# Optimization experiments

Hardware: AMD Instinct MI355X
Metric: run time of the kernel (lower is better)

The kernel has to match this reference:

```python
import jax, jax.numpy as jnp
import numpy as np

B, P1, P2 = 32, 25, 24          # batch, patch rows (+1 cls row), patch cols
D1, D2, D3 = 8, 8, 12           # factored embed dims (total d = 768)
H1, H2, H3 = 2, 2, 4            # factored heads (16 total)
X, Y, Z = D1 // H1, D2 // H2, D3 // H3   # per-head factor dims -> head dim 48
SCALE = float((X * Y * Z) ** -0.5)


def tle(x, w1, w2, w3, b):
    # Tensor Linear Embedding: mode-wise linear maps on the last 3 modes + bias.
    return jnp.einsum('bpqijk,ai,cj,dk->bpqacd', x, w1, w2, w3) + b


def split_heads(t):
    # (b,p1,p2,(x h1),(y h2),(z h3)) -> (b,h1,h2,h3, p1*p2, x*y*z)
    b, p1, p2, _, _, _ = t.shape
    t = t.reshape(b, p1, p2, X, H1, Y, H2, Z, H3)
    t = t.transpose(0, 4, 6, 8, 1, 2, 3, 5, 7)
    return t.reshape(b, H1, H2, H3, p1 * p2, X * Y * Z)


def merge_heads(t, p1, p2):
    # (b,h1,h2,h3,S,D) -> (b,p1,p2,(x h1),(y h2),(z h3))
    b = t.shape[0]
    t = t.reshape(b, H1, H2, H3, p1, p2, X, Y, Z)
    t = t.transpose(0, 4, 5, 6, 1, 7, 2, 8, 3)
    return t.reshape(b, p1, p2, X * H1, Y * H2, Z * H3)


def setup_inputs() -> dict:
    key = jax.random.key(0)
    ks = jax.random.split(key, 20)

    def w(k, shape):
        return jax.random.normal(k, shape, jnp.float32) * 0.02

    inp = {"x": jax.random.normal(ks[0], (B, P1, P2, D1, D2, D3), jnp.float32)}
    for i, n in enumerate(["q", "k", "v", "o"]):
        inp[f"w{n}1"] = w(ks[1 + 4 * i], (D1, D1))
        inp[f"w{n}2"] = w(ks[2 + 4 * i], (D2, D2))
        inp[f"w{n}3"] = w(ks[3 + 4 * i], (D3, D3))
        inp[f"b{n}"] = w(ks[4 + 4 * i], (D1, D2, D3))
    return inp


def reference(x, wq1, wq2, wq3, bq, wk1, wk2, wk3, bk,
              wv1, wv2, wv3, bv, wo1, wo2, wo3, bo):
    q = split_heads(tle(x, wq1, wq2, wq3, bq))
    k = split_heads(tle(x, wk1, wk2, wk3, bk))
    v = split_heads(tle(x, wv1, wv2, wv3, bv))
    # scores: (b,h1,h2,h3,S,S) with S = 600
    attn = jax.nn.softmax(jnp.einsum('befgsd,befgtd->befgst', q, k) * SCALE, axis=-1)
    o = jnp.einsum('befgst,befgtd->befgsd', attn, v)
    o = merge_heads(o, P1, P2)
    return tle(o, wo1, wo2, wo3, bo)
```

## Files before the change

kernel.cpp:

```cpp
#include <hip/hip_runtime.h>
#include <hip/hip_bf16.h>
#include <cstdint>

#define Bc    32
#define Sc    600
#define NHc   16
#define SP    640
#define NKT   19
#define DHc   48
#define DP    64
#define SCALEc 0.14433756729740643f

typedef __bf16   bf16x8 __attribute__((ext_vector_type(8)));
typedef float    f32x4  __attribute__((ext_vector_type(4)));
typedef float    f32x16 __attribute__((ext_vector_type(16)));
typedef uint32_t u32x4  __attribute__((ext_vector_type(4)));

static __device__ __forceinline__ f32x16 mfma32(bf16x8 a, bf16x8 b, f32x16 c) {
    return __builtin_amdgcn_mfma_f32_32x32x16_bf16(a, b, c, 0, 0, 0);
}
static __device__ __forceinline__ unsigned short f2bf(float f) {
    uint32_t u = __builtin_bit_cast(uint32_t, f);
    u += 0x7FFFu + ((u >> 16) & 1u);
    return (unsigned short)(u >> 16);
}
static __device__ __forceinline__ f32x16 fzero16() {
    f32x16 z;
    #pragma unroll
    for (int i = 0; i < 16; ++i) z[i] = 0.f;
    return z;
}
static __device__ __forceinline__ void gload_lds16(const void* g, void* l) {
    __builtin_amdgcn_global_load_lds(
        (const __attribute__((address_space(1))) unsigned int*)g,
        (__attribute__((address_space(3))) unsigned int*)l, 16, 0, 0);
}

__global__ __launch_bounds__(256) void tle_qkv(
    const float* __restrict__ x,
    const float* __restrict__ wq1, const float* __restrict__ wq2,
    const float* __restrict__ wq3, const float* __restrict__ bq,
    const float* __restrict__ wk1, const float* __restrict__ wk2,
    const float* __restrict__ wk3, const float* __restrict__ bk,
    const float* __restrict__ wv1, const float* __restrict__ wv2,
    const float* __restrict__ wv3, const float* __restrict__ bv,
    __hip_bfloat16* __restrict__ Qb, __hip_bfloat16* __restrict__ Kb,
    __hip_bfloat16* __restrict__ Vr)
{
    __shared__ __align__(16) float xs[768];
    __shared__ __align__(16) float t1s[3][8][100];
    __shared__ __align__(16) float w3s[3][144];
    __shared__ __align__(16) unsigned short outs[3][16][64];
    const int t = threadIdx.x;
    const int patch = blockIdx.x;
    const int b = patch / Sc, s = patch - b * Sc;
    if (t < 192) ((float4*)xs)[t] = ((const float4*)(x + (size_t)patch * 768))[t];
    if (t < 144) { w3s[0][t] = wq3[t]; w3s[1][t] = wk3[t]; w3s[2][t] = wv3[t]; }
    __syncthreads();

    const int pr = t >> 6, a = (t >> 3) & 7, c = t & 7;
    float w2r[8];
    if (t < 192) {
        const float* w1 = pr == 0 ? wq1 : pr == 1 ? wk1 : wv1;
        const float* w2 = pr == 0 ? wq2 : pr == 1 ? wk2 : wv2;
        float w1r[8];
        #pragma unroll
        for (int i = 0; i < 8; ++i) w1r[i] = w1[a*8 + i];
        #pragma unroll
        for (int j = 0; j < 8; ++j) w2r[j] = w2[c*8 + j];
        float s1[12];
        #pragma unroll
        for (int k = 0; k < 12; ++k) s1[k] = 0.f;
        #pragma unroll
        for (int i = 0; i < 8; ++i) {
            const float4* xr = (const float4*)&xs[i*96 + c*12];
            float4 v0 = xr[0], v1 = xr[1], v2 = xr[2];
            float wv = w1r[i];
            s1[0] += wv*v0.x; s1[1] += wv*v0.y; s1[2]  += wv*v0.z; s1[3]  += wv*v0.w;
            s1[4] += wv*v1.x; s1[5] += wv*v1.y; s1[6]  += wv*v1.z; s1[7]  += wv*v1.w;
            s1[8] += wv*v2.x; s1[9] += wv*v2.y; s1[10] += wv*v2.z; s1[11] += wv*v2.w;
        }
        float4* tw = (float4*)&t1s[pr][a][c*12];
        tw[0] = make_float4(s1[0], s1[1], s1[2],  s1[3]);
        tw[1] = make_float4(s1[4], s1[5], s1[6],  s1[7]);
        tw[2] = make_float4(s1[8], s1[9], s1[10], s1[11]);
    }
    __syncthreads();
    if (t < 192) {
        float t2r[12];
        #pragma unroll
        for (int k = 0; k < 12; ++k) t2r[k] = 0.f;
        #pragma unroll
        for (int j = 0; j < 8; ++j) {
            const float4* tr = (const float4*)&t1s[pr][a][j*12];
            float4 v0 = tr[0], v1 = tr[1], v2 = tr[2];
            float wv = w2r[j];
            t2r[0] += wv*v0.x; t2r[1] += wv*v0.y; t2r[2]  += wv*v0.z; t2r[3]  += wv*v0.w;
            t2r[4] += wv*v1.x; t2r[5] += wv*v1.y; t2r[6]  += wv*v1.z; t2r[7]  += wv*v1.w;
            t2r[8] += wv*v2.x; t2r[9] += wv*v2.y; t2r[10] += wv*v2.z; t2r[11] += wv*v2.w;
        }
        const float* bb = pr == 0 ? bq : pr == 1 ? bk : bv;
        const float4* bp = (const float4*)(bb + a*96 + c*12);
        float4 b0 = bp[0], b1 = bp[1], b2 = bp[2];
        float bias_[12] = {b0.x,b0.y,b0.z,b0.w, b1.x,b1.y,b1.z,b1.w, b2.x,b2.y,b2.z,b2.w};
        #pragma unroll
        for (int d = 0; d < 12; ++d) {
            const float4* wr = (const float4*)&w3s[pr][d*12];
            float4 u0 = wr[0], u1 = wr[1], u2 = wr[2];
            float od = bias_[d]
                + t2r[0]*u0.x + t2r[1]*u0.y + t2r[2] *u0.z + t2r[3] *u0.w
                + t2r[4]*u1.x + t2r[5]*u1.y + t2r[6] *u1.z + t2r[7] *u1.w
                + t2r[8]*u2.x + t2r[9]*u2.y + t2r[10]*u2.z + t2r[11]*u2.w;
            if (pr == 0) od *= SCALEc;
            int h  = (a & 1)*8 + (c & 1)*4 + (d & 3);
            int dh = (a >> 1)*12 + (c >> 1)*3 + (d >> 2);
            outs[pr][h][dh] = f2bf(od);
        }
    }
    if (t < 96) {
        int prr = t >> 5, rem = t & 31, h = rem >> 1, half = rem & 1;
        *(uint4*)&outs[prr][h][48 + half*8] = make_uint4(0u, 0u, 0u, 0u);
    }
    __syncthreads();
    for (int u = t; u < 384; u += 256) {
        int prr = u >> 7, rem = u & 127, h = rem >> 3, u8 = rem & 7;
        __hip_bfloat16* dstp = prr == 0 ? Qb : prr == 1 ? Kb : Vr;
        uint4 v = *(const uint4*)&outs[prr][h][u8*8];
        *(uint4*)(dstp + ((size_t)(b*NHc + h) * SP + s) * DP + u8*8) = v;
    }
}

__global__ __launch_bounds__(256) void vtrans(
    const __hip_bfloat16* __restrict__ Vr, __hip_bfloat16* __restrict__ Vt,
    __hip_bfloat16* __restrict__ Kb)
{
    __shared__ __align__(16) short Ls[64][72];
    const int t = threadIdx.x;
    const int bh = blockIdx.x, st = blockIdx.y;
    const __hip_bfloat16* src = Vr + ((size_t)bh * SP + st*64) * DP;
    for (int u = t; u < 512; u += 256) {
        int r = u >> 3, c = (u & 7) * 8;
        *(bf16x8*)&Ls[r][c] = *(const bf16x8*)(src + (size_t)r * DP + c);
    }
    __syncthreads();
    const unsigned short one_bf = 0x3F80;
    for (int u = t; u < 384; u += 256) {
        int dh = u >> 3, cb = (u & 7) * 8;
        int gcol = st*64 + cb;
        if (gcol >= Sc + 8) continue;
        union { unsigned short s[8]; bf16x8 v; } o;
        if (gcol >= Sc) {
            #pragma unroll
            for (int j = 0; j < 8; ++j) o.s[j] = 0;
        } else {
            #pragma unroll
            for (int j = 0; j < 8; ++j) o.s[j] = (unsigned short)Ls[cb + j][dh];
        }
        *(bf16x8*)(Vt + ((size_t)bh*64 + dh) * SP + st*64 + cb) = o.v;
    }
    if (t < 128) {
        int r = 48 + (t >> 3), cb = (t & 7) * 8;
        union { unsigned short s[8]; bf16x8 v; } o;
        #pragma unroll
        for (int j = 0; j < 8; ++j) {
            int col = st*64 + cb + j;
            o.s[j] = (r == 48 && col < Sc) ? one_bf : (unsigned short)0;
        }
        *(bf16x8*)(Vt + ((size_t)bh*64 + r) * SP + st*64 + cb) = o.v;
    }
    if (st == 9 && t < 64) {
        int r = 600 + (t >> 3), cb = (t & 7) * 8;
        union { unsigned short s[8]; bf16x8 v; } z;
        #pragma unroll
        for (int j = 0; j < 8; ++j) z.s[j] = 0;
        *(bf16x8*)(Kb + ((size_t)bh * SP + r) * DP + cb) = z.v;
    }
}

static __device__ __forceinline__ void softmax_pack(
    const f32x16& sv, bf16x8& pf0, bf16x8& pf1)
{
    float p[16];
    #pragma unroll
    for (int r = 0; r < 16; ++r) p[r] = __expf(sv[r]);
    uint32_t Wa0, Wa1, Wa2, Wa3, Wb0, Wb1, Wb2, Wb3;
    asm("v_cvt_pk_bf16_f32 %0, %1, %2" : "=v"(Wa0) : "v"(p[0]),  "v"(p[1]));
    asm("v_cvt_pk_bf16_f32 %0, %1, %2" : "=v"(Wb0) : "v"(p[2]),  "v"(p[3]));
    asm("v_cvt_pk_bf16_f32 %0, %1, %2" : "=v"(Wa1) : "v"(p[4]),  "v"(p[5]));
    asm("v_cvt_pk_bf16_f32 %0, %1, %2" : "=v"(Wb1) : "v"(p[6]),  "v"(p[7]));
    asm("v_cvt_pk_bf16_f32 %0, %1, %2" : "=v"(Wa2) : "v"(p[8]),  "v"(p[9]));
    asm("v_cvt_pk_bf16_f32 %0, %1, %2" : "=v"(Wb2) : "v"(p[10]), "v"(p[11]));
    asm("v_cvt_pk_bf16_f32 %0, %1, %2" : "=v"(Wa3) : "v"(p[12]), "v"(p[13]));
    asm("v_cvt_pk_bf16_f32 %0, %1, %2" : "=v"(Wb3) : "v"(p[14]), "v"(p[15]));
    asm("v_permlane32_swap_b32 %0, %1" : "+v"(Wa0), "+v"(Wa1));
    asm("v_permlane32_swap_b32 %0, %1" : "+v"(Wb0), "+v"(Wb1));
    asm("v_permlane32_swap_b32 %0, %1" : "+v"(Wa2), "+v"(Wa3));
    asm("v_permlane32_swap_b32 %0, %1" : "+v"(Wb2), "+v"(Wb3));
    pf0 = __builtin_bit_cast(bf16x8, (u32x4){Wa0, Wb0, Wa1, Wb1});
    pf1 = __builtin_bit_cast(bf16x8, (u32x4){Wa2, Wb2, Wa3, Wb3});
}

__global__ __launch_bounds__(64, 2) void attn_mfma(
    const __hip_bfloat16* __restrict__ Qb, const __hip_bfloat16* __restrict__ Kb,
    const __hip_bfloat16* __restrict__ Vt, float* __restrict__ Ob)
{
    __shared__ __align__(16) char Ks[2][4096];
    __shared__ __align__(16) char Vs[2][4096];
    const int l = threadIdx.x;
    const int q32 = l & 31, hl = l >> 5;
    const int bid = blockIdx.x;
    const int lg = (bid & 7) * 320 + (bid >> 3);
    const int bh = lg / 5, qb = lg - bh * 5;
    const int b = bh >> 4, h = bh & 15;

    const char* Kbh = (const char*)(Kb + (size_t)bh * SP * DP);
    const char* Vbh = (const char*)(Vt + (size_t)bh * 64 * SP);

    const int krow = l >> 3;
    const char* ksrc = Kbh + krow*128 + (((l & 7)*16) ^ (krow << 4));
    const char* vsrc = Vbh + (size_t)(l >> 2)*(SP*2) + (l & 3)*16;

    bf16x8 qf[4][3];
    #pragma unroll
    for (int f = 0; f < 4; ++f) {
        const __hip_bfloat16* Qp = Qb + ((size_t)bh*SP + qb*128 + f*32 + q32) * DP;
        #pragma unroll
        for (int ck = 0; ck < 3; ++ck)
            qf[f][ck] = *(const bf16x8*)(Qp + ck*16 + hl*8);
    }
    f32x16 acc[4][2];
    #pragma unroll
    for (int f = 0; f < 4; ++f) { acc[f][0] = fzero16(); acc[f][1] = fzero16(); }

    auto stage = [&](int kt, int bfi) {
        const char* ks = ksrc + (size_t)kt * 4096;
        const char* vs = vsrc + (size_t)kt * 64;
        #pragma unroll
        for (int i = 0; i < 4; ++i)
            gload_lds16(ks + i*1024, &Ks[bfi][i*1024]);
        #pragma unroll
        for (int i = 0; i < 4; ++i)
            gload_lds16(vs + (size_t)i*16*(SP*2), &Vs[bfi][i*1024]);
    };

    stage(0, 0);
    int bfi = 0;
    #pragma unroll 1
    for (int kt = 0; kt < NKT; ++kt) {
        asm volatile("s_waitcnt vmcnt(0)" ::: "memory");
        __builtin_amdgcn_sched_barrier(0);
        bf16x8 kf[3], vf[2][2];
        #pragma unroll
        for (int ck = 0; ck < 3; ++ck)
            kf[ck] = *(const bf16x8*)&Ks[bfi][q32*128 + ((ck*32 + hl*16) ^ ((q32 & 7) << 4))];
        #pragma unroll
        for (int db = 0; db < 2; ++db)
            #pragma unroll
            for (int c2 = 0; c2 < 2; ++c2)
                vf[db][c2] = *(const bf16x8*)&Vs[bfi][(db*32 + q32)*64 + c2*32 + hl*16];
        if (kt + 1 < NKT) stage(kt + 1, bfi ^ 1);
        __builtin_amdgcn_s_setprio(1);
        #pragma unroll
        for (int f = 0; f < 4; ++f) {
            f32x16 s = fzero16();
            s = mfma32(kf[0], qf[f][0], s);
            s = mfma32(kf[1], qf[f][1], s);
            s = mfma32(kf[2], qf[f][2], s);
            bf16x8 pf0, pf1;
            softmax_pack(s, pf0, pf1);
            acc[f][0] = mfma32(vf[0][0], pf0, acc[f][0]);
            acc[f][0] = mfma32(vf[0][1], pf1, acc[f][0]);
            acc[f][1] = mfma32(vf[1][0], pf0, acc[f][1]);
            acc[f][1] = mfma32(vf[1][1], pf1, acc[f][1]);
        }
        __builtin_amdgcn_s_setprio(0);
        bfi ^= 1;
    }

    #pragma unroll
    for (int f = 0; f < 4; ++f) {
        float ls = acc[f][1][8];
        float other = __shfl_xor(ls, 32);
        float tot = hl ? other : ls;
        float inv = 1.f / tot;
        int q = qb*128 + f*32 + q32;
        if (q < Sc) {
            float* orow = Ob + ((size_t)b*Sc + q)*768 + h*48;
            #pragma unroll
            for (int rq = 0; rq < 4; ++rq) {
                int d0 = rq*8 + hl*4;
                float4 v4 = make_float4(acc[f][0][rq*4+0]*inv, acc[f][0][rq*4+1]*inv,
                                        acc[f][0][rq*4+2]*inv, acc[f][0][rq*4+3]*inv);
                *(float4*)(orow + d0) = v4;
            }
            #pragma unroll
            for (int rq = 0; rq < 2; ++rq) {
                int d0 = 32 + rq*8 + hl*4;
                float4 v4 = make_float4(acc[f][1][rq*4+0]*inv, acc[f][1][rq*4+1]*inv,
                                        acc[f][1][rq*4+2]*inv, acc[f][1][rq*4+3]*inv);
                *(float4*)(orow + d0) = v4;
            }
        }
    }
}

__global__ __launch_bounds__(256) void tle_out(
    const float* __restrict__ Oin, const float* __restrict__ w1g,
    const float* __restrict__ w2g, const float* __restrict__ w3g,
    const float* __restrict__ bias, float* __restrict__ out)
{
    __shared__ __align__(16) float xs[4][768];
    __shared__ __align__(16) float t1s[4][8][100];
    __shared__ __align__(16) float w3s[144];
    const int t = threadIdx.x;
    const int p4 = t >> 6, a = (t >> 3) & 7, c = t & 7;
    const int lane = t & 63;
    const int patch = blockIdx.x * 4 + p4;
    for (int o4 = lane; o4 < 192; o4 += 64) {
        float4 v = *(const float4*)(Oin + (size_t)patch * 768 + o4*4);
        int h = o4 / 12, r = o4 - h*12;
        #pragma unroll
        for (int q = 0; q < 4; ++q) {
            int dh = r*4 + q;
            int xq = dh / 12, rem2 = dh - xq*12, yq = rem2 / 3, zq = rem2 - yq*3;
            int aa = xq*2 + (h >> 3), cc = yq*2 + ((h >> 2) & 1), dd = zq*4 + (h & 3);
            xs[p4][aa*96 + cc*12 + dd] = ((const float*)&v)[q];
        }
    }
    if (t < 144) w3s[t] = w3g[t];
    __syncthreads();
    float w2r[8];
    {
        float w1r[8];
        #pragma unroll
        for (int i = 0; i < 8; ++i) w1r[i] = w1g[a*8 + i];
        #pragma unroll
        for (int j = 0; j < 8; ++j) w2r[j] = w2g[c*8 + j];
        float s1[12];
        #pragma unroll
        for (int k = 0; k < 12; ++k) s1[k] = 0.f;
        #pragma unroll
        for (int i = 0; i < 8; ++i) {
            const float4* xr = (const float4*)&xs[p4][i*96 + c*12];
            float4 v0 = xr[0], v1 = xr[1], v2 = xr[2];
            float wv = w1r[i];
            s1[0] += wv*v0.x; s1[1] += wv*v0.y; s1[2]  += wv*v0.z; s1[3]  += wv*v0.w;
            s1[4] += wv*v1.x; s1[5] += wv*v1.y; s1[6]  += wv*v1.z; s1[7]  += wv*v1.w;
            s1[8] += wv*v2.x; s1[9] += wv*v2.y; s1[10] += wv*v2.z; s1[11] += wv*v2.w;
        }
        float4* tw = (float4*)&t1s[p4][a][c*12];
        tw[0] = make_float4(s1[0], s1[1], s1[2],  s1[3]);
        tw[1] = make_float4(s1[4], s1[5], s1[6],  s1[7]);
        tw[2] = make_float4(s1[8], s1[9], s1[10], s1[11]);
    }
    __syncthreads();
    {
        float t2r[12];
        #pragma unroll
        for (int k = 0; k < 12; ++k) t2r[k] = 0.f;
        #pragma unroll
        for (int j = 0; j < 8; ++j) {
            const float4* tr = (const float4*)&t1s[p4][a][j*12];
            float4 v0 = tr[0], v1 = tr[1], v2 = tr[2];
            float wv = w2r[j];
            t2r[0] += wv*v0.x; t2r[1] += wv*v0.y; t2r[2]  += wv*v0.z; t2r[3]  += wv*v0.w;
            t2r[4] += wv*v1.x; t2r[5] += wv*v1.y; t2r[6]  += wv*v1.z; t2r[7]  += wv*v1.w;
            t2r[8] += wv*v2.x; t2r[9] += wv*v2.y; t2r[10] += wv*v2.z; t2r[11] += wv*v2.w;
        }
        const float4* bp = (const float4*)(bias + a*96 + c*12);
        float4 b0 = bp[0], b1 = bp[1], b2 = bp[2];
        float bias_[12] = {b0.x,b0.y,b0.z,b0.w, b1.x,b1.y,b1.z,b1.w, b2.x,b2.y,b2.z,b2.w};
        float od[12];
        #pragma unroll
        for (int d = 0; d < 12; ++d) {
            const float4* wr = (const float4*)&w3s[d*12];
            float4 u0 = wr[0], u1 = wr[1], u2 = wr[2];
            od[d] = bias_[d]
                + t2r[0]*u0.x + t2r[1]*u0.y + t2r[2] *u0.z + t2r[3] *u0.w
                + t2r[4]*u1.x + t2r[5]*u1.y + t2r[6] *u1.z + t2r[7] *u1.w
                + t2r[8]*u2.x + t2r[9]*u2.y + t2r[10]*u2.z + t2r[11]*u2.w;
        }
        float4* op = (float4*)(out + (size_t)patch*768 + a*96 + c*12);
        op[0] = make_float4(od[0], od[1], od[2],  od[3]);
        op[1] = make_float4(od[4], od[5], od[6],  od[7]);
        op[2] = make_float4(od[8], od[9], od[10], od[11]);
    }
}

extern "C" void kernel_launch(void* const* d_in, const int* in_sizes, int n_in,
                              void* d_out, int out_size, void* d_ws, size_t ws_size,
                              hipStream_t stream) {
    const float* x   = (const float*)d_in[0];
    const float* wq1 = (const float*)d_in[1];
    const float* wq2 = (const float*)d_in[2];
    const float* wq3 = (const float*)d_in[3];
    const float* bq  = (const float*)d_in[4];
    const float* wk1 = (const float*)d_in[5];
    const float* wk2 = (const float*)d_in[6];
    const float* wk3 = (const float*)d_in[7];
    const float* bk  = (const float*)d_in[8];
    const float* wv1 = (const float*)d_in[9];
    const float* wv2 = (const float*)d_in[10];
    const float* wv3 = (const float*)d_in[11];
    const float* bv  = (const float*)d_in[12];
    const float* wo1 = (const float*)d_in[13];
    const float* wo2 = (const float*)d_in[14];
    const float* wo3 = (const float*)d_in[15];
    const float* bo  = (const float*)d_in[16];
    float* out = (float*)d_out;

    char* ws = (char*)d_ws;
    const size_t SZ_QK = (size_t)512 * SP * DP * 2;
    __hip_bfloat16* Qb = (__hip_bfloat16*)ws;
    __hip_bfloat16* Kb = (__hip_bfloat16*)(ws + SZ_QK);
    __hip_bfloat16* Vr = (__hip_bfloat16*)(ws + 2*SZ_QK);
    __hip_bfloat16* Vt = (__hip_bfloat16*)(ws + 3*SZ_QK);
    float*          Ob = (float*)(ws + 4*SZ_QK);

    dim3 blk(256);
    tle_qkv<<<Bc*Sc, blk, 0, stream>>>(x, wq1, wq2, wq3, bq,
                                       wk1, wk2, wk3, bk,
                                       wv1, wv2, wv3, bv, Qb, Kb, Vr);
    vtrans<<<dim3(512, 10), blk, 0, stream>>>(Vr, Vt, Kb);
    attn_mfma<<<2560, 64, 0, stream>>>(Qb, Kb, Vt, Ob);
    tle_out<<<Bc*Sc/4, blk, 0, stream>>>(Ob, wo1, wo2, wo3, bo, out);
}
```

Before: 197.9 us.

## Process four patches per block in QKV embedding and store intermediates as bf16

The QKV tensor embedding now handles four patches per 256-thread block instead of one, with each thread computing the Q, K and V projections together so x is read from shared memory once for all three. The intermediate t1 buffer in shared memory is packed to bf16 in both TLE kernels, and the w3 weights are read straight from global memory instead of being staged in shared memory. The aim is to cut the number of blocks, the idle threads (previously 64 of 256 were unused) and shared-memory traffic. The extra bf16 rounding of the intermediate adds precision loss, and holding more registers per thread may lower occupancy.

Result: no change. 195.7 us (-1.1%).

```diff
diff --git a/kernel.cpp b/kernel.cpp
--- a/kernel.cpp
+++ b/kernel.cpp
@@ -23,6 +23,9 @@
     uint32_t u = __builtin_bit_cast(uint32_t, f);
     u += 0x7FFFu + ((u >> 16) & 1u);
     return (unsigned short)(u >> 16);
+}
+static __device__ __forceinline__ float bfbits(uint32_t w, int odd) {
+    return __builtin_bit_cast(float, odd ? (w & 0xffff0000u) : (w << 16));
 }
 static __device__ __forceinline__ f32x16 fzero16() {
     f32x16 z;
@@ -47,65 +50,98 @@
     __hip_bfloat16* __restrict__ Qb, __hip_bfloat16* __restrict__ Kb,
     __hip_bfloat16* __restrict__ Vr)
 {
-    __shared__ __align__(16) float xs[768];
-    __shared__ __align__(16) float t1s[3][8][100];
-    __shared__ __align__(16) float w3s[3][144];
-    __shared__ __align__(16) unsigned short outs[3][16][64];
+    __shared__ __align__(16) float xs[4][768];
+    __shared__ __align__(16) unsigned short t1s[3][4][8][104];
+    __shared__ __align__(16) unsigned short outs[4][3][16][64];
     const int t = threadIdx.x;
-    const int patch = blockIdx.x;
-    const int b = patch / Sc, s = patch - b * Sc;
-    if (t < 192) ((float4*)xs)[t] = ((const float4*)(x + (size_t)patch * 768))[t];
-    if (t < 144) { w3s[0][t] = wq3[t]; w3s[1][t] = wk3[t]; w3s[2][t] = wv3[t]; }
-    __syncthreads();
-
-    const int pr = t >> 6, a = (t >> 3) & 7, c = t & 7;
-    float w2r[8];
-    if (t < 192) {
+    const int p = t >> 6, a = (t >> 3) & 7, c = t & 7;
+    const int patch0 = blockIdx.x * 4;
+
+    {
+        const float4* xg = (const float4*)(x + (size_t)patch0 * 768);
+        float4* xl = (float4*)xs;
+        xl[t] = xg[t]; xl[t + 256] = xg[t + 256]; xl[t + 512] = xg[t + 512];
+    }
+    float w1r[3][8], w2r[3][8];
+    #pragma unroll
+    for (int pr = 0; pr < 3; ++pr) {
         const float* w1 = pr == 0 ? wq1 : pr == 1 ? wk1 : wv1;
         const float* w2 = pr == 0 ? wq2 : pr == 1 ? wk2 : wv2;
-        float w1r[8];
-        #pragma unroll
-        for (int i = 0; i < 8; ++i) w1r[i] = w1[a*8 + i];
-        #pragma unroll
-        for (int j = 0; j < 8; ++j) w2r[j] = w2[c*8 + j];
-        float s1[12];
-        #pragma unroll
-        for (int k = 0; k < 12; ++k) s1[k] = 0.f;
-        #pragma unroll
-        for (int i = 0; i < 8; ++i) {
-            const float4* xr = (const float4*)&xs[i*96 + c*12];
-            float4 v0 = xr[0], v1 = xr[1], v2 = xr[2];
-            float wv = w1r[i];
-            s1[0] += wv*v0.x; s1[1] += wv*v0.y; s1[2]  += wv*v0.z; s1[3]  += wv*v0.w;
-            s1[4] += wv*v1.x; s1[5] += wv*v1.y; s1[6]  += wv*v1.z; s1[7]  += wv*v1.w;
-            s1[8] += wv*v2.x; s1[9] += wv*v2.y; s1[10] += wv*v2.z; s1[11] += wv*v2.w;
-        }
-        float4* tw = (float4*)&t1s[pr][a][c*12];
-        tw[0] = make_float4(s1[0], s1[1], s1[2],  s1[3]);
-        tw[1] = make_float4(s1[4], s1[5], s1[6],  s1[7]);
-        tw[2] = make_float4(s1[8], s1[9], s1[10], s1[11]);
-    }
-    __syncthreads();
-    if (t < 192) {
+        #pragma unroll
+        for (int i = 0; i < 8; ++i) { w1r[pr][i] = w1[a*8 + i]; w2r[pr][i] = w2[c*8 + i]; }
+    }
+    __syncthreads();
+
+    float s1[3][12];
+    #pragma unroll
+    for (int pr = 0; pr < 3; ++pr)
+        #pragma unroll
+        for (int k = 0; k < 12; ++k) s1[pr][k] = 0.f;
+    #pragma unroll
+    for (int i = 0; i < 8; ++i) {
+        const float4* xr = (const float4*)&xs[p][i*96 + c*12];
+        float4 v0 = xr[0], v1 = xr[1], v2 = xr[2];
+        #pragma unroll
+        for (int pr = 0; pr < 3; ++pr) {
+            float wv = w1r[pr][i];
+            s1[pr][0] += wv*v0.x; s1[pr][1] += wv*v0.y; s1[pr][2]  += wv*v0.z; s1[pr][3]  += wv*v0.w;
+            s1[pr][4] += wv*v1.x; s1[pr][5] += wv*v1.y; s1[pr][6]  += wv*v1.z; s1[pr][7]  += wv*v1.w;
+            s1[pr][8] += wv*v2.x; s1[pr][9] += wv*v2.y; s1[pr][10] += wv*v2.z; s1[pr][11] += wv*v2.w;
+        }
+    }
+    #pragma unroll
+    for (int pr = 0; pr < 3; ++pr) {
+        uint32_t pk[6];
+        #pragma unroll
+        for (int n = 0; n < 6; ++n)
+            asm("v_cvt_pk_bf16_f32 %0, %1, %2" : "=v"(pk[n])
+                : "v"(s1[pr][2*n]), "v"(s1[pr][2*n+1]));
+        unsigned short* row = &t1s[pr][p][a][0];
+        *(uint2*)(row + c*12 + 0) = make_uint2(pk[0], pk[1]);
+        *(uint2*)(row + c*12 + 4) = make_uint2(pk[2], pk[3]);
+        *(uint2*)(row + c*12 + 8) = make_uint2(pk[4], pk[5]);
+    }
+    {
+        int u = t;
+        int pp = u / 96, r = u - pp*96, pr = r >> 5, r2 = r & 31, h = r2 >> 1, half = r2 & 1;
+        *(uint4*)&outs[pp][pr][h][48 + half*8] = make_uint4(0u,0u,0u,0u);
+        u = t + 256;
+        if (u < 384) {
+            pp = u / 96; r = u - pp*96; pr = r >> 5; r2 = r & 31; h = r2 >> 1; half = r2 & 1;
+            *(uint4*)&outs[pp][pr][h][48 + half*8] = make_uint4(0u,0u,0u,0u);
+        }
+    }
+    __syncthreads();
+
+    #pragma unroll
+    for (int pr = 0; pr < 3; ++pr) {
+        uint4 q[12];
+        const uint4* t1p = (const uint4*)&t1s[pr][p][a][0];
+        #pragma unroll
+        for (int n = 0; n < 12; ++n) q[n] = t1p[n];
         float t2r[12];
         #pragma unroll
         for (int k = 0; k < 12; ++k) t2r[k] = 0.f;
         #pragma unroll
         for (int j = 0; j < 8; ++j) {
-            const float4* tr = (const float4*)&t1s[pr][a][j*12];
-            float4 v0 = tr[0], v1 = tr[1], v2 = tr[2];
-            float wv = w2r[j];
-            t2r[0] += wv*v0.x; t2r[1] += wv*v0.y; t2r[2]  += wv*v0.z; t2r[3]  += wv*v0.w;
-            t2r[4] += wv*v1.x; t2r[5] += wv*v1.y; t2r[6]  += wv*v1.z; t2r[7]  += wv*v1.w;
-            t2r[8] += wv*v2.x; t2r[9] += wv*v2.y; t2r[10] += wv*v2.z; t2r[11] += wv*v2.w;
-        }
-        const float* bb = pr == 0 ? bq : pr == 1 ? bk : bv;
+            float wv = w2r[pr][j];
+            #pragma unroll
+            for (int k = 0; k < 12; ++k) {
+                int idx = j*12 + k;
+                uint32_t w = ((const uint32_t*)&q[idx >> 2])[idx & 3 ? 0 : 0];
+                uint32_t ww = __builtin_bit_cast(u32x4, q[idx >> 3])[ (idx >> 1) & 3 ];
+                (void)w;
+                t2r[k] += wv * bfbits(ww, idx & 1);
+            }
+        }
+        const float* w3p = pr == 0 ? wq3 : pr == 1 ? wk3 : wv3;
+        const float* bb  = pr == 0 ? bq  : pr == 1 ? bk  : bv;
         const float4* bp = (const float4*)(bb + a*96 + c*12);
         float4 b0 = bp[0], b1 = bp[1], b2 = bp[2];
         float bias_[12] = {b0.x,b0.y,b0.z,b0.w, b1.x,b1.y,b1.z,b1.w, b2.x,b2.y,b2.z,b2.w};
         #pragma unroll
         for (int d = 0; d < 12; ++d) {
-            const float4* wr = (const float4*)&w3s[pr][d*12];
+            const float4* wr = (const float4*)(w3p + d*12);
             float4 u0 = wr[0], u1 = wr[1], u2 = wr[2];
             float od = bias_[d]
                 + t2r[0]*u0.x + t2r[1]*u0.y + t2r[2] *u0.z + t2r[3] *u0.w
@@ -114,18 +150,19 @@
             if (pr == 0) od *= SCALEc;
             int h  = (a & 1)*8 + (c & 1)*4 + (d & 3);
             int dh = (a >> 1)*12 + (c >> 1)*3 + (d >> 2);
-            outs[pr][h][dh] = f2bf(od);
-        }
-    }
-    if (t < 96) {
-        int prr = t >> 5, rem = t & 31, h = rem >> 1, half = rem & 1;
-        *(uint4*)&outs[prr][h][48 + half*8] = make_uint4(0u, 0u, 0u, 0u);
-    }
-    __syncthreads();
-    for (int u = t; u < 384; u += 256) {
-        int prr = u >> 7, rem = u & 127, h = rem >> 3, u8 = rem & 7;
-        __hip_bfloat16* dstp = prr == 0 ? Qb : prr == 1 ? Kb : Vr;
-        uint4 v = *(const uint4*)&outs[prr][h][u8*8];
+            outs[p][pr][h][dh] = f2bf(od);
+        }
+    }
+    __syncthreads();
+
+    #pragma unroll
+    for (int rep = 0; rep < 6; ++rep) {
+        int u = t + rep*256;
+        int pp = u / 384, r = u - pp*384, pr = r >> 7, r2 = r & 127, h = r2 >> 3, u8 = r2 & 7;
+        uint4 v = *(const uint4*)&outs[pp][pr][h][u8*8];
+        __hip_bfloat16* dstp = pr == 0 ? Qb : pr == 1 ? Kb : Vr;
+        int patch = patch0 + pp;
+        int b = patch / Sc, s = patch - b * Sc;
         *(uint4*)(dstp + ((size_t)(b*NHc + h) * SP + s) * DP + u8*8) = v;
     }
 }
@@ -310,12 +347,11 @@
     const float* __restrict__ bias, float* __restrict__ out)
 {
     __shared__ __align__(16) float xs[4][768];
-    __shared__ __align__(16) float t1s[4][8][100];
-    __shared__ __align__(16) float w3s[144];
+    __shared__ __align__(16) unsigned short t1s[4][8][104];
     const int t = threadIdx.x;
-    const int p4 = t >> 6, a = (t >> 3) & 7, c = t & 7;
+    const int p = t >> 6, a = (t >> 3) & 7, c = t & 7;
     const int lane = t & 63;
-    const int patch = blockIdx.x * 4 + p4;
+    const int patch = blockIdx.x * 4 + p;
     for (int o4 = lane; o4 < 192; o4 += 64) {
         float4 v = *(const float4*)(Oin + (size_t)patch * 768 + o4*4);
         int h = o4 / 12, r = o4 - h*12;
@@ -324,67 +360,73 @@
             int dh = r*4 + q;
             int xq = dh / 12, rem2 = dh - xq*12, yq = rem2 / 3, zq = rem2 - yq*3;
             int aa = xq*2 + (h >> 3), cc = yq*2 + ((h >> 2) & 1), dd = zq*4 + (h & 3);
-            xs[p4][aa*96 + cc*12 + dd] = ((const float*)&v)[q];
-        }
-    }
-    if (t < 144) w3s[t] = w3g[t];
-    __syncthreads();
-    float w2r[8];
+            xs[p][aa*96 + cc*12 + dd] = ((const float*)&v)[q];
+        }
+    }
+    float w1r[8], w2r[8];
+    #pragma unroll
+    for (int i = 0; i < 8; ++i) { w1r[i] = w1g[a*8 + i]; w2r[i] = w2g[c*8 + i]; }
+    __syncthreads();
+
+    float s1[12];
+    #pragma unroll
+    for (int k = 0; k < 12; ++k) s1[k] = 0.f;
+    #pragma unroll
+    for (int i = 0; i < 8; ++i) {
+        const float4* xr = (const float4*)&xs[p][i*96 + c*12];
+        float4 v0 = xr[0], v1 = xr[1], v2 = xr[2];
+        float wv = w1r[i];
+        s1[0] += wv*v0.x; s1[1] += wv*v0.y; s1[2]  += wv*v0.z; s1[3]  += wv*v0.w;
+        s1[4] += wv*v1.x; s1[5] += wv*v1.y; s1[6]  += wv*v1.z; s1[7]  += wv*v1.w;
+        s1[8] += wv*v2.x; s1[9] += wv*v2.y; s1[10] += wv*v2.z; s1[11] += wv*v2.w;
+    }
     {
-        float w1r[8];
-        #pragma unroll
-        for (int i = 0; i < 8; ++i) w1r[i] = w1g[a*8 + i];
-        #pragma unroll
-        for (int j = 0; j < 8; ++j) w2r[j] = w2g[c*8 + j];
-        float s1[12];
-        #pragma unroll
-        for (int k = 0; k < 12; ++k) s1[k] = 0.f;
-        #pragma unroll
-        for (int i = 0; i < 8; ++i) {
-            const float4* xr = (const float4*)&xs[p4][i*96 + c*12];
-            float4 v0 = xr[0], v1 = xr[1], v2 = xr[2];
-            float wv = w1r[i];
-            s1[0] += wv*v0.x; s1[1] += wv*v0.y; s1[2]  += wv*v0.z; s1[3]  += wv*v0.w;
-            s1[4] += wv*v1.x; s1[5] += wv*v1.y; s1[6]  += wv*v1.z; s1[7]  += wv*v1.w;
-            s1[8] += wv*v2.x; s1[9] += wv*v2.y; s1[10] += wv*v2.z; s1[11] += wv*v2.w;
-        }
-        float4* tw = (float4*)&t1s[p4][a][c*12];
-        tw[0] = make_float4(s1[0], s1[1], s1[2],  s1[3]);
-        tw[1] = make_float4(s1[4], s1[5], s1[6],  s1[7]);
-        tw[2] = make_float4(s1[8], s1[9], s1[10], s1[11]);
-    }
-    __syncthreads();
-    {
-        float t2r[12];
-        #pragma unroll
-        for (int k = 0; k < 12; ++k) t2r[k] = 0.f;
-        #pragma unroll
-        for (int j = 0; j < 8; ++j) {
-            const float4* tr = (const float4*)&t1s[p4][a][j*12];
-            float4 v0 = tr[0], v1 = tr[1], v2 = tr[2];
-            float wv = w2r[j];
-            t2r[0] += wv*v0.x; t2r[1] += wv*v0.y; t2r[2]  += wv*v0.z; t2r[3]  += wv*v0.w;
-            t2r[4] += wv*v1.x; t2r[5] += wv*v1.y; t2r[6]  += wv*v1.z; t2r[7]  += wv*v1.w;
-            t2r[8] += wv*v2.x; t2r[9] += wv*v2.y; t2r[10] += wv*v2.z; t2r[11] += wv*v2.w;
-        }
-        const float4* bp = (const float4*)(bias + a*96 + c*12);
-        float4 b0 = bp[0], b1 = bp[1], b2 = bp[2];
-        float bias_[12] = {b0.x,b0.y,b0.z,b0.w, b1.x,b1.y,b1.z,b1.w, b2.x,b2.y,b2.z,b2.w};
-        float od[12];
-        #pragma unroll
-        for (int d = 0; d < 12; ++d) {
-            const float4* wr = (const float4*)&w3s[d*12];
-            float4 u0 = wr[0], u1 = wr[1], u2 = wr[2];
-            od[d] = bias_[d]
-                + t2r[0]*u0.x + t2r[1]*u0.y + t2r[2] *u0.z + t2r[3] *u0.w
-                + t2r[4]*u1.x + t2r[5]*u1.y + t2r[6] *u1.z + t2r[7] *u1.w
-                + t2r[8]*u2.x + t2r[9]*u2.y + t2r[10]*u2.z + t2r[11]*u2.w;
-        }
-        float4* op = (float4*)(out + (size_t)patch*768 + a*96 + c*12);
-        op[0] = make_float4(od[0], od[1], od[2],  od[3]);
-        op[1] = make_float4(od[4], od[5], od[6],  od[7]);
-        op[2] = make_float4(od[8], od[9], od[10], od[11]);
-    }
+        uint32_t pk[6];
+        #pragma unroll
+        for (int n = 0; n < 6; ++n)
+            asm("v_cvt_pk_bf16_f32 %0, %1, %2" : "=v"(pk[n])
+                : "v"(s1[2*n]), "v"(s1[2*n+1]));
+        unsigned short* row = &t1s[p][a][0];
+        *(uint2*)(row + c*12 + 0) = make_uint2(pk[0], pk[1]);
+        *(uint2*)(row + c*12 + 4) = make_uint2(pk[2], pk[3]);
+        *(uint2*)(row + c*12 + 8) = make_uint2(pk[4], pk[5]);
+    }
+    __syncthreads();
+
+    uint4 q[12];
+    const uint4* t1p = (const uint4*)&t1s[p][a][0];
+    #pragma unroll
+    for (int n = 0; n < 12; ++n) q[n] = t1p[n];
+    float t2r[12];
+    #pragma unroll
+    for (int k = 0; k < 12; ++k) t2r[k] = 0.f;
+    #pragma unroll
+    for (int j = 0; j < 8; ++j) {
+        float wv = w2r[j];
+        #pragma unroll
+        for (int k = 0; k < 12; ++k) {
+            int idx = j*12 + k;
+            uint32_t ww = __builtin_bit_cast(u32x4, q[idx >> 3])[(idx >> 1) & 3];
+            t2r[k] += wv * bfbits(ww, idx & 1);
+        }
+    }
+    const float4* bp = (const float4*)(bias + a*96 + c*12);
+    float4 b0 = bp[0], b1 = bp[1], b2 = bp[2];
+    float bias_[12] = {b0.x,b0.y,b0.z,b0.w, b1.x,b1.y,b1.z,b1.w, b2.x,b2.y,b2.z,b2.w};
+    float od[12];
+    #pragma unroll
+    for (int d = 0; d < 12; ++d) {
+        const float4* wr = (const float4*)(w3g + d*12);
+        float4 u0 = wr[0], u1 = wr[1], u2 = wr[2];
+        od[d] = bias_[d]
+            + t2r[0]*u0.x + t2r[1]*u0.y + t2r[2] *u0.z + t2r[3] *u0.w
+            + t2r[4]*u1.x + t2r[5]*u1.y + t2r[6] *u1.z + t2r[7] *u1.w
+            + t2r[8]*u2.x + t2r[9]*u2.y + t2r[10]*u2.z + t2r[11]*u2.w;
+    }
+    float4* op = (float4*)(out + (size_t)patch*768 + a*96 + c*12);
+    op[0] = make_float4(od[0], od[1], od[2],  od[3]);
+    op[1] = make_float4(od[4], od[5], od[6],  od[7]);
+    op[2] = make_float4(od[8], od[9], od[10], od[11]);
 }
 
 extern "C" void kernel_launch(void* const* d_in, const int* in_sizes, int n_in,
@@ -418,9 +460,9 @@
     float*          Ob = (float*)(ws + 4*SZ_QK);
 
     dim3 blk(256);
-    tle_qkv<<<Bc*Sc, blk, 0, stream>>>(x, wq1, wq2, wq3, bq,
-                                       wk1, wk2, wk3, bk,
-                                       wv1, wv2, wv3, bv, Qb, Kb, Vr);
+    tle_qkv<<<Bc*Sc/4, blk, 0, stream>>>(x, wq1, wq2, wq3, bq,
+                                         wk1, wk2, wk3, bk,
+                                         wv1, wv2, wv3, bv, Qb, Kb, Vr);
     vtrans<<<dim3(512, 10), blk, 0, stream>>>(Vr, Vt, Kb);
     attn_mfma<<<2560, 64, 0, stream>>>(Qb, Kb, Vt, Ob);
     tle_out<<<Bc*Sc/4, blk, 0, stream>>>(Ob, wo1, wo2, wo3, bo, out);
```
